# Kernel tuning notes

Hardware: AMD Instinct MI355X
Metric: run time of the kernel (lower is better)

The kernel has to match this reference:

```python
import jax, jax.numpy as jnp
import numpy as np

D_MODEL = 1024
N_HEADS = 16
HEAD_DIM = 64
N_KV_HEADS = 4
D_FF = 4096
LN_EPS = 1e-5


def setup_inputs() -> dict:
    key = jax.random.key(0)
    ks = jax.random.split(key, 10)
    s = lambda fan_in: 1.0 / np.sqrt(fan_in)
    return {
        "x": jax.random.normal(ks[0], (2, 2048, D_MODEL), dtype=jnp.float32),
        "ln_w": jnp.ones((D_MODEL,), dtype=jnp.float32),
        "ln_b": jnp.zeros((D_MODEL,), dtype=jnp.float32),
        # Linear weights stored as (in, out): y = x @ W
        "wq": jax.random.normal(ks[1], (D_MODEL, N_HEADS * HEAD_DIM), dtype=jnp.float32) * s(D_MODEL),
        "wk": jax.random.normal(ks[2], (D_MODEL, N_KV_HEADS * HEAD_DIM), dtype=jnp.float32) * s(D_MODEL),
        "wv": jax.random.normal(ks[3], (D_MODEL, N_KV_HEADS * HEAD_DIM), dtype=jnp.float32) * s(D_MODEL),
        "wo": jax.random.normal(ks[4], (N_HEADS * HEAD_DIM, D_MODEL), dtype=jnp.float32) * s(N_HEADS * HEAD_DIM),
        "w_gate": jax.random.normal(ks[5], (D_MODEL, D_FF), dtype=jnp.float32) * s(D_MODEL),
        "w_up": jax.random.normal(ks[6], (D_MODEL, D_FF), dtype=jnp.float32) * s(D_MODEL),
        "w_down": jax.random.normal(ks[7], (D_FF, D_MODEL), dtype=jnp.float32) * s(D_FF),
    }


def _layernorm(x, w, b):
    mu = jnp.mean(x, axis=-1, keepdims=True)
    var = jnp.var(x, axis=-1, keepdims=True)
    return (x - mu) * jax.lax.rsqrt(var + LN_EPS) * w + b


def _attention(normed, wq, wk, wv, wo):
    B, S, _ = normed.shape
    h, kh, hd = N_HEADS, N_KV_HEADS, HEAD_DIM
    groups = h // kh
    scale = 1.0 / np.sqrt(hd)
    q = (normed @ wq).reshape(B, S, h, hd).transpose(0, 2, 1, 3)   # [B,h,S,hd]
    k = (normed @ wk).reshape(B, S, kh, hd).transpose(0, 2, 1, 3)  # [B,kh,S,hd]
    v = (normed @ wv).reshape(B, S, kh, hd).transpose(0, 2, 1, 3)
    if groups != 1:
        # matches torch repeat_interleave along head dim
        k = jnp.repeat(k, groups, axis=1)
        v = jnp.repeat(v, groups, axis=1)
    scores = jnp.einsum("bhqd,bhkd->bhqk", q, k) * scale
    causal = jnp.tril(jnp.ones((S, S), dtype=bool))
    scores = jnp.where(causal, scores, -jnp.inf)
    attn = jax.nn.softmax(scores, axis=-1)
    out = jnp.einsum("bhqk,bhkd->bhqd", attn, v)
    out = out.transpose(0, 2, 1, 3).reshape(B, S, h * hd)
    return out @ wo


def _ffn(normed, w_gate, w_up, w_down):
    return (jax.nn.silu(normed @ w_gate) * (normed @ w_up)) @ w_down


def reference(x, ln_w, ln_b, wq, wk, wv, wo, w_gate, w_up, w_down):
    normed = _layernorm(x, ln_w, ln_b)
    attn_out = _attention(normed, wq, wk, wv, wo)
    ffn_out = _ffn(normed, w_gate, w_up, w_down)
    return x + attn_out + ffn_out
```

## Files before the change

kernel.cpp:

```cpp
#include <hip/hip_runtime.h>
#include <cstdint>

typedef __bf16 bf16x8 __attribute__((ext_vector_type(8)));
typedef float f32x4 __attribute__((ext_vector_type(4)));
typedef float f32x16 __attribute__((ext_vector_type(16)));
typedef unsigned short u16;

#define MFMA16(a, b, c) __builtin_amdgcn_mfma_f32_16x16x32_bf16((a), (b), (c), 0, 0, 0)
#define MFMA32(a, b, c) __builtin_amdgcn_mfma_f32_32x32x16_bf16((a), (b), (c), 0, 0, 0)

#define GLLDS(gp, lp) __builtin_amdgcn_global_load_lds( \
    (const __attribute__((address_space(1))) uint32_t*)(gp), \
    (__attribute__((address_space(3))) uint32_t*)(lp), 16, 0, 0)

__device__ __forceinline__ u16 f2bf(float f) {
    union { float f; uint32_t u; } v; v.f = f;
    uint32_t u = v.u;
    u += 0x7FFFu + ((u >> 16) & 1u);
    return (u16)(u >> 16);
}
__device__ __forceinline__ float bf2f(u16 h) {
    union { uint32_t u; float f; } v; v.u = ((uint32_t)h) << 16;
    return v.f;
}

__global__ __launch_bounds__(256) void transpose_cast(const float* __restrict__ in,
                                                      u16* __restrict__ out, int R, int C) {
    __shared__ float tile[32][33];
    int c0 = blockIdx.x * 32, r0 = blockIdx.y * 32;
    int tx = threadIdx.x & 31, ty = threadIdx.x >> 5;
#pragma unroll
    for (int i = ty; i < 32; i += 8)
        tile[i][tx] = in[(size_t)(r0 + i) * C + c0 + tx];
    __syncthreads();
#pragma unroll
    for (int i = ty; i < 32; i += 8)
        out[(size_t)(c0 + i) * R + r0 + tx] = f2bf(tile[tx][i]);
}

__global__ __launch_bounds__(256) void transpose_v(const u16* __restrict__ in, u16* __restrict__ out,
                                                   int in_stride) {
    __shared__ u16 tile[32][33];
    int b = blockIdx.z;
    int c0 = blockIdx.x * 32, s0 = blockIdx.y * 32;
    int tx = threadIdx.x & 31, ty = threadIdx.x >> 5;
#pragma unroll
    for (int i = ty; i < 32; i += 8)
        tile[i][tx] = in[(size_t)(b * 2048 + s0 + i) * in_stride + c0 + tx];
    __syncthreads();
#pragma unroll
    for (int i = ty; i < 32; i += 8)
        out[(size_t)b * 256 * 2048 + (size_t)(c0 + i) * 2048 + s0 + tx] = tile[tx][i];
}

__global__ __launch_bounds__(256) void ln_kernel(const float* __restrict__ x,
                                                 const float* __restrict__ w,
                                                 const float* __restrict__ bb,
                                                 u16* __restrict__ normed) {
    int row = blockIdx.x;
    int tid = threadIdx.x;
    float4 v = ((const float4*)(x + (size_t)row * 1024))[tid];
    float s = v.x + v.y + v.z + v.w;
    float s2 = v.x * v.x + v.y * v.y + v.z * v.z + v.w * v.w;
#pragma unroll
    for (int off = 1; off < 64; off <<= 1) {
        s += __shfl_xor(s, off);
        s2 += __shfl_xor(s2, off);
    }
    __shared__ float rs[4], rs2[4];
    int wv = tid >> 6;
    if ((tid & 63) == 0) { rs[wv] = s; rs2[wv] = s2; }
    __syncthreads();
    s = rs[0] + rs[1] + rs[2] + rs[3];
    s2 = rs2[0] + rs2[1] + rs2[2] + rs2[3];
    float mu = s * (1.0f / 1024.0f);
    float var = s2 * (1.0f / 1024.0f) - mu * mu;
    float inv = rsqrtf(var + 1e-5f);
    float4 wv4 = ((const float4*)w)[tid];
    float4 bv4 = ((const float4*)bb)[tid];
    ushort4 o;
    o.x = f2bf((v.x - mu) * inv * wv4.x + bv4.x);
    o.y = f2bf((v.y - mu) * inv * wv4.y + bv4.y);
    o.z = f2bf((v.z - mu) * inv * wv4.z + bv4.z);
    o.w = f2bf((v.w - mu) * inv * wv4.w + bv4.w);
    *(ushort4*)(normed + (size_t)row * 1024 + tid * 4) = o;
}

__global__ __launch_bounds__(256) void gemm_bt64(const u16* __restrict__ A, const u16* __restrict__ Bt,
                                                 void* __restrict__ Cv,
                                                 const float* __restrict__ xres,
                                                 int N, int K, int mode) {
    __shared__ __align__(16) u16 As[128 * 64];
    __shared__ __align__(16) u16 Bs[64 * 64];
    const int tid = threadIdx.x, lane = tid & 63, wv = tid >> 6;
    const int row0 = blockIdx.x * 128, col0 = blockIdx.y * 64;
    const int wr = (wv >> 1) * 64, wc = (wv & 1) * 32;
    const int fr = lane & 15, fg = lane >> 4;
    const int lr8 = lane >> 3;
    const int lc8s = ((lane & 7) ^ lr8) * 8;

    f32x4 acc[4][2];
#pragma unroll
    for (int i = 0; i < 4; ++i)
#pragma unroll
        for (int j = 0; j < 2; ++j) acc[i][j] = (f32x4){0.f, 0.f, 0.f, 0.f};

    const u16* ga = A + (size_t)(row0 + 32 * wv + lr8) * K + lc8s;
    const u16* gb = Bt + (size_t)(col0 + 16 * wv + lr8) * K + lc8s;
    u16* la = As + wv * 2048;
    u16* lb = Bs + wv * 1024;
    const int f7 = fr & 7;

    for (int k0 = 0; k0 < K; k0 += 64) {
        __syncthreads();
        GLLDS(ga + k0, la);
        GLLDS(ga + (size_t)8 * K + k0, la + 512);
        GLLDS(ga + (size_t)16 * K + k0, la + 1024);
        GLLDS(ga + (size_t)24 * K + k0, la + 1536);
        GLLDS(gb + k0, lb);
        GLLDS(gb + (size_t)8 * K + k0, lb + 512);
        __syncthreads();
#pragma unroll
        for (int kk = 0; kk < 2; ++kk) {
            bf16x8 af[4], bfr[2];
#pragma unroll
            for (int i = 0; i < 4; ++i)
                af[i] = *(const bf16x8*)(As + (wr + i * 16 + fr) * 64 + (((kk * 4 + fg) ^ f7) * 8));
#pragma unroll
            for (int j = 0; j < 2; ++j)
                bfr[j] = *(const bf16x8*)(Bs + (wc + j * 16 + fr) * 64 + (((kk * 4 + fg) ^ f7) * 8));
#pragma unroll
            for (int i = 0; i < 4; ++i)
#pragma unroll
                for (int j = 0; j < 2; ++j)
                    acc[i][j] = MFMA16(af[i], bfr[j], acc[i][j]);
        }
    }

    if (mode == 0) {
        u16* C = (u16*)Cv;
#pragma unroll
        for (int i = 0; i < 4; ++i)
#pragma unroll
            for (int j = 0; j < 2; ++j)
#pragma unroll
                for (int r = 0; r < 4; ++r) {
                    int row = row0 + wr + i * 16 + fg * 4 + r;
                    int col = col0 + wc + j * 16 + fr;
                    C[(size_t)row * N + col] = f2bf(acc[i][j][r]);
                }
    } else if (mode == 1) {
        float* C = (float*)Cv;
#pragma unroll
        for (int i = 0; i < 4; ++i)
#pragma unroll
            for (int j = 0; j < 2; ++j)
#pragma unroll
                for (int r = 0; r < 4; ++r) {
                    int row = row0 + wr + i * 16 + fg * 4 + r;
                    int col = col0 + wc + j * 16 + fr;
                    C[(size_t)row * N + col] = acc[i][j][r];
                }
    } else {
        float* C = (float*)Cv;
#pragma unroll
        for (int i = 0; i < 4; ++i)
#pragma unroll
            for (int j = 0; j < 2; ++j)
#pragma unroll
                for (int r = 0; r < 4; ++r) {
                    int row = row0 + wr + i * 16 + fg * 4 + r;
                    int col = col0 + wc + j * 16 + fr;
                    size_t off = (size_t)row * N + col;
                    C[off] = acc[i][j][r] + xres[off];
                }
    }
}

__global__ __launch_bounds__(256) void gemm_gateup(const u16* __restrict__ A,
                                                   const u16* __restrict__ Bg,
                                                   const u16* __restrict__ Bu,
                                                   u16* __restrict__ H, int N, int K) {
    __shared__ __align__(16) u16 As[128 * 64];
    __shared__ __align__(16) u16 Bgs[64 * 64];
    __shared__ __align__(16) u16 Bus[64 * 64];
    const int tid = threadIdx.x, lane = tid & 63, wv = tid >> 6;
    const int row0 = blockIdx.x * 128, col0 = blockIdx.y * 64;
    const int wr = (wv >> 1) * 64, wc = (wv & 1) * 32;
    const int fr = lane & 15, fg = lane >> 4;
    const int lr8 = lane >> 3;
    const int lc8s = ((lane & 7) ^ lr8) * 8;

    f32x4 ag[4][2], au[4][2];
#pragma unroll
    for (int i = 0; i < 4; ++i)
#pragma unroll
        for (int j = 0; j < 2; ++j) {
            ag[i][j] = (f32x4){0.f, 0.f, 0.f, 0.f};
            au[i][j] = (f32x4){0.f, 0.f, 0.f, 0.f};
        }

    const u16* ga = A + (size_t)(row0 + 32 * wv + lr8) * K + lc8s;
    const u16* gg = Bg + (size_t)(col0 + 16 * wv + lr8) * K + lc8s;
    const u16* gu = Bu + (size_t)(col0 + 16 * wv + lr8) * K + lc8s;
    u16* la = As + wv * 2048;
    u16* lg = Bgs + wv * 1024;
    u16* lu = Bus + wv * 1024;
    const int f7 = fr & 7;

    for (int k0 = 0; k0 < K; k0 += 64) {
        __syncthreads();
        GLLDS(ga + k0, la);
        GLLDS(ga + (size_t)8 * K + k0, la + 512);
        GLLDS(ga + (size_t)16 * K + k0, la + 1024);
        GLLDS(ga + (size_t)24 * K + k0, la + 1536);
        GLLDS(gg + k0, lg);
        GLLDS(gg + (size_t)8 * K + k0, lg + 512);
        GLLDS(gu + k0, lu);
        GLLDS(gu + (size_t)8 * K + k0, lu + 512);
        __syncthreads();
#pragma unroll
        for (int kk = 0; kk < 2; ++kk) {
            bf16x8 af[4], bg[2], bu[2];
#pragma unroll
            for (int i = 0; i < 4; ++i)
                af[i] = *(const bf16x8*)(As + (wr + i * 16 + fr) * 64 + (((kk * 4 + fg) ^ f7) * 8));
#pragma unroll
            for (int j = 0; j < 2; ++j) {
                bg[j] = *(const bf16x8*)(Bgs + (wc + j * 16 + fr) * 64 + (((kk * 4 + fg) ^ f7) * 8));
                bu[j] = *(const bf16x8*)(Bus + (wc + j * 16 + fr) * 64 + (((kk * 4 + fg) ^ f7) * 8));
            }
#pragma unroll
            for (int i = 0; i < 4; ++i)
#pragma unroll
                for (int j = 0; j < 2; ++j) {
                    ag[i][j] = MFMA16(af[i], bg[j], ag[i][j]);
                    au[i][j] = MFMA16(af[i], bu[j], au[i][j]);
                }
        }
    }

#pragma unroll
    for (int i = 0; i < 4; ++i)
#pragma unroll
        for (int j = 0; j < 2; ++j)
#pragma unroll
            for (int r = 0; r < 4; ++r) {
                int row = row0 + wr + i * 16 + fg * 4 + r;
                int col = col0 + wc + j * 16 + fr;
                float g = ag[i][j][r];
                float sg = g / (1.0f + __expf(-g));
                H[(size_t)row * N + col] = f2bf(sg * au[i][j][r]);
            }
}

__global__ __launch_bounds__(512) void attn_kernel(const u16* __restrict__ qkv,
                                                   const u16* __restrict__ Vt,
                                                   u16* __restrict__ Ob) {
    __shared__ __align__(16) u16 Ks[2][64 * 64];
    __shared__ __align__(16) u16 Vs[2][64 * 64];
    const int tid = threadIdx.x, lane = tid & 63, w = tid >> 6;
    const int bid = blockIdx.x;
    const int qblk = 7 - (bid & 7);
    const int h = (bid >> 3) & 15;
    const int b = bid >> 7;
    const int kh = h >> 2;
    const int q0 = qblk * 256;
    const int lo = lane & 31, hi = lane >> 5;
    const int qg = q0 + w * 32 + lo;
    const int S = 2048, QS = 1536;

    bf16x8 qf[4];
    {
        const u16* qrow = qkv + (size_t)(b * S + qg) * QS + h * 64 + 8 * hi;
        qf[0] = *(const bf16x8*)(qrow);
        qf[1] = *(const bf16x8*)(qrow + 16);
        qf[2] = *(const bf16x8*)(qrow + 32);
        qf[3] = *(const bf16x8*)(qrow + 48);
    }

    f32x16 o0 = {}, o1 = {};
    float mr = -1e30f, ls = 0.f;
    const int nt = (q0 >> 6) + 4;
    const int wq0 = q0 + w * 32;

    const int sr = w * 8 + (lane >> 3);
    const int scb = ((lane & 7) ^ (sr & 7)) * 8;
    const u16* kg = qkv + (size_t)b * S * QS + 1024 + kh * 64 + scb;
    const u16* vg = Vt + (size_t)(b * 4 + kh) * 64 * 2048 + (size_t)sr * 2048 + scb;
    u16* lk = (u16*)Ks + w * 512;
    u16* lv = (u16*)Vs + w * 512;

#define STAGE(buf, t) { const int kv0s = (t) * 64; \
    GLLDS(kg + (size_t)(kv0s + sr) * QS, lk + (buf) * 4096); \
    GLLDS(vg + kv0s, lv + (buf) * 4096); }

    STAGE(0, 0)
    asm volatile("s_waitcnt vmcnt(0)" ::: "memory");
    __syncthreads();

    const int lrow = lo * 64;
    const int l7 = lo & 7;

    for (int t = 0; t < nt; ++t) {
        const int cur = t & 1;
        if (t + 1 < nt) STAGE(cur ^ 1, t + 1)
        const int kv0 = t * 64;
        if (kv0 <= wq0 + 31) {
            const u16* KB = (const u16*)Ks + cur * 4096;
            const u16* VB = (const u16*)Vs + cur * 4096;
            f32x16 sc0 = {}, sc1 = {};
#pragma unroll
            for (int ds = 0; ds < 4; ++ds) {
                bf16x8 kf0 = *(const bf16x8*)(KB + lrow + (((2 * ds + hi) ^ l7) * 8));
                sc0 = MFMA32(kf0, qf[ds], sc0);
                bf16x8 kf1 = *(const bf16x8*)(KB + 2048 + lrow + (((2 * ds + hi) ^ l7) * 8));
                sc1 = MFMA32(kf1, qf[ds], sc1);
            }

            float xv[32];
            if (kv0 + 63 <= wq0) {
#pragma unroll
                for (int i = 0; i < 16; ++i) {
                    xv[i] = sc0[i] * 0.125f;
                    xv[16 + i] = sc1[i] * 0.125f;
                }
            } else {
#pragma unroll
                for (int i = 0; i < 16; ++i) {
                    int k0g = kv0 + (i & 3) + 8 * (i >> 2) + 4 * hi;
                    xv[i]      = (k0g      <= qg) ? sc0[i] * 0.125f : -1e30f;
                    xv[16 + i] = (k0g + 32 <= qg) ? sc1[i] * 0.125f : -1e30f;
                }
            }
            float m = xv[0];
#pragma unroll
            for (int i = 1; i < 32; ++i) m = fmaxf(m, xv[i]);
            m = fmaxf(m, __shfl_xor(m, 32));
            float nm = fmaxf(mr, m);
            float al = __expf(mr - nm);
            mr = nm;
            float sum = 0.f;
#pragma unroll
            for (int i = 0; i < 32; ++i) {
                float p = __expf(xv[i] - nm);
                xv[i] = p;
                sum += p;
            }
            sum += __shfl_xor(sum, 32);
            ls = ls * al + sum;
#pragma unroll
            for (int i = 0; i < 16; ++i) { o0[i] *= al; o1[i] *= al; }

            bf16x8 pf[4];
#pragma unroll
            for (int g = 0; g < 4; ++g) {
                uint32_t w0, w1, w2, w3;
                asm("v_cvt_pk_bf16_f32 %0, %1, %2" : "=v"(w0) : "v"(xv[g * 8 + 0]), "v"(xv[g * 8 + 1]));
                asm("v_cvt_pk_bf16_f32 %0, %1, %2" : "=v"(w1) : "v"(xv[g * 8 + 2]), "v"(xv[g * 8 + 3]));
                asm("v_cvt_pk_bf16_f32 %0, %1, %2" : "=v"(w2) : "v"(xv[g * 8 + 4]), "v"(xv[g * 8 + 5]));
                asm("v_cvt_pk_bf16_f32 %0, %1, %2" : "=v"(w3) : "v"(xv[g * 8 + 6]), "v"(xv[g * 8 + 7]));
                asm volatile("v_permlane32_swap_b32 %0, %1" : "+v"(w0), "+v"(w2));
                asm volatile("v_permlane32_swap_b32 %0, %1" : "+v"(w1), "+v"(w3));
                union { uint32_t u[4]; bf16x8 v; } pk;
                pk.u[0] = w0; pk.u[1] = w1; pk.u[2] = w2; pk.u[3] = w3;
                pf[g] = pk.v;
            }

#pragma unroll
            for (int ks = 0; ks < 4; ++ks) {
                bf16x8 vf0 = *(const bf16x8*)(VB + lrow + (((2 * ks + hi) ^ l7) * 8));
                o0 = MFMA32(vf0, pf[ks], o0);
                bf16x8 vf1 = *(const bf16x8*)(VB + 2048 + lrow + (((2 * ks + hi) ^ l7) * 8));
                o1 = MFMA32(vf1, pf[ks], o1);
            }
        }
        asm volatile("s_waitcnt vmcnt(0)" ::: "memory");
        __syncthreads();
    }
#undef STAGE

    const float inv = 1.0f / ls;
    u16* orow = Ob + (size_t)(b * S + qg) * 1024 + h * 64;
#pragma unroll
    for (int rg = 0; rg < 4; ++rg) {
        ushort4 w4;
        w4.x = f2bf(o0[rg * 4 + 0] * inv);
        w4.y = f2bf(o0[rg * 4 + 1] * inv);
        w4.z = f2bf(o0[rg * 4 + 2] * inv);
        w4.w = f2bf(o0[rg * 4 + 3] * inv);
        *(ushort4*)(orow + rg * 8 + 4 * hi) = w4;
        w4.x = f2bf(o1[rg * 4 + 0] * inv);
        w4.y = f2bf(o1[rg * 4 + 1] * inv);
        w4.z = f2bf(o1[rg * 4 + 2] * inv);
        w4.w = f2bf(o1[rg * 4 + 3] * inv);
        *(ushort4*)(orow + 32 + rg * 8 + 4 * hi) = w4;
    }
}

extern "C" void kernel_launch(void* const* d_in, const int* in_sizes, int n_in,
                              void* d_out, int out_size, void* d_ws, size_t ws_size,
                              hipStream_t stream) {
    const float* x    = (const float*)d_in[0];
    const float* ln_w = (const float*)d_in[1];
    const float* ln_b = (const float*)d_in[2];
    const float* wq   = (const float*)d_in[3];
    const float* wk   = (const float*)d_in[4];
    const float* wv   = (const float*)d_in[5];
    const float* wo   = (const float*)d_in[6];
    const float* wg   = (const float*)d_in[7];
    const float* wu   = (const float*)d_in[8];
    const float* wd   = (const float*)d_in[9];
    float* out = (float*)d_out;

    char* ws = (char*)d_ws;
    u16* QKVT   = (u16*)(ws + 0x0000000);
    u16* WOT    = (u16*)(ws + 0x0300000);
    u16* WGT    = (u16*)(ws + 0x0500000);
    u16* WUT    = (u16*)(ws + 0x0D00000);
    u16* WDT    = (u16*)(ws + 0x1500000);
    u16* NORMED = (u16*)(ws + 0x1D00000);
    u16* QKV    = (u16*)(ws + 0x2500000);
    u16* VT     = (u16*)(ws + 0x3100000);
    u16* ATTN   = (u16*)(ws + 0x3300000);
    float* P1   = (float*)(ws + 0x3B00000);
    u16* Hb     = (u16*)(ws + 0x4B00000);

    transpose_cast<<<dim3(32, 32), 256, 0, stream>>>(wq, QKVT, 1024, 1024);
    transpose_cast<<<dim3(8, 32), 256, 0, stream>>>(wk, QKVT + (size_t)1024 * 1024, 1024, 256);
    transpose_cast<<<dim3(8, 32), 256, 0, stream>>>(wv, QKVT + (size_t)1280 * 1024, 1024, 256);
    transpose_cast<<<dim3(32, 32), 256, 0, stream>>>(wo, WOT, 1024, 1024);
    transpose_cast<<<dim3(128, 32), 256, 0, stream>>>(wg, WGT, 1024, 4096);
    transpose_cast<<<dim3(128, 32), 256, 0, stream>>>(wu, WUT, 1024, 4096);
    transpose_cast<<<dim3(32, 128), 256, 0, stream>>>(wd, WDT, 4096, 1024);

    ln_kernel<<<4096, 256, 0, stream>>>(x, ln_w, ln_b, NORMED);

    gemm_bt64<<<dim3(32, 24), 256, 0, stream>>>(NORMED, QKVT, QKV, nullptr, 1536, 1024, 0);
    transpose_v<<<dim3(8, 64, 2), 256, 0, stream>>>(QKV + 1280, VT, 1536);
    attn_kernel<<<256, 512, 0, stream>>>(QKV, VT, ATTN);
    gemm_bt64<<<dim3(32, 16), 256, 0, stream>>>(ATTN, WOT, P1, x, 1024, 1024, 4);

    gemm_gateup<<<dim3(32, 64), 256, 0, stream>>>(NORMED, WGT, WUT, Hb, 4096, 1024);
    gemm_bt64<<<dim3(32, 16), 256, 0, stream>>>(Hb, WDT, out, P1, 1024, 4096, 4);
}
```

Baseline: 290.2 us.

## Interleave gate/up weights and use 256x256 double-buffered 8-wave gate-up GEMM

Gate and up weights are transposed into one interleaved matrix (16-column groups alternating gate/up), so a single B stream feeds both products. The gate-up GEMM becomes a 256x256 tile, 512-thread kernel with double-buffered LDS, prefetch split across phases, and setprio around MFMA bursts. The aim is more data reuse per tile and overlap of global loads with compute. In exchange it uses much more LDS and registers (128 accumulator floats per lane) and launches only 512 blocks, which limits occupancy.

```diff
diff --git a/kernel.cpp b/kernel.cpp
--- a/kernel.cpp
+++ b/kernel.cpp
@@ -36,6 +36,23 @@
 #pragma unroll
     for (int i = ty; i < 32; i += 8)
         out[(size_t)(c0 + i) * R + r0 + tx] = f2bf(tile[tx][i]);
+}
+
+__global__ __launch_bounds__(256) void transpose_cast_gu(const float* __restrict__ in,
+                                                         u16* __restrict__ out, int upflag) {
+    __shared__ float tile[32][33];
+    int c0 = blockIdx.x * 32, r0 = blockIdx.y * 32;
+    int tx = threadIdx.x & 31, ty = threadIdx.x >> 5;
+#pragma unroll
+    for (int i = ty; i < 32; i += 8)
+        tile[i][tx] = in[(size_t)(r0 + i) * 4096 + c0 + tx];
+    __syncthreads();
+#pragma unroll
+    for (int i = ty; i < 32; i += 8) {
+        int n = c0 + i;
+        int orow = ((n >> 4) << 5) + (n & 15) + upflag * 16;
+        out[(size_t)orow * 1024 + r0 + tx] = f2bf(tile[tx][i]);
+    }
 }
 
 __global__ __launch_bounds__(256) void transpose_v(const u16* __restrict__ in, u16* __restrict__ out,
@@ -177,80 +194,126 @@
     }
 }
 
-__global__ __launch_bounds__(256) void gemm_gateup(const u16* __restrict__ A,
-                                                   const u16* __restrict__ Bg,
-                                                   const u16* __restrict__ Bu,
-                                                   u16* __restrict__ H, int N, int K) {
-    __shared__ __align__(16) u16 As[128 * 64];
-    __shared__ __align__(16) u16 Bgs[64 * 64];
-    __shared__ __align__(16) u16 Bus[64 * 64];
-    const int tid = threadIdx.x, lane = tid & 63, wv = tid >> 6;
-    const int row0 = blockIdx.x * 128, col0 = blockIdx.y * 64;
-    const int wr = (wv >> 1) * 64, wc = (wv & 1) * 32;
-    const int fr = lane & 15, fg = lane >> 4;
-    const int lr8 = lane >> 3;
-    const int lc8s = ((lane & 7) ^ lr8) * 8;
-
-    f32x4 ag[4][2], au[4][2];
-#pragma unroll
-    for (int i = 0; i < 4; ++i)
-#pragma unroll
-        for (int j = 0; j < 2; ++j) {
-            ag[i][j] = (f32x4){0.f, 0.f, 0.f, 0.f};
-            au[i][j] = (f32x4){0.f, 0.f, 0.f, 0.f};
+__global__ __launch_bounds__(512, 2) void gemm_wgu_8ph(const u16* __restrict__ A,
+                                                       const u16* __restrict__ Bp,
+                                                       u16* __restrict__ H) {
+    __shared__ __align__(16) u16 As[2][256 * 64];
+    __shared__ __align__(16) u16 Bs[2][256 * 64];
+    const int tid = threadIdx.x, lane = tid & 63, w = tid >> 6;
+    const int wm = w >> 2, wn = w & 3;
+    const int row0 = blockIdx.x * 256;
+    const int col0 = blockIdx.y * 256;
+    const int fr = lane & 15, fg = lane >> 4, f7 = fr & 7;
+    const int K = 1024;
+    const int nk = 16;
+
+    f32x4 acc[8][4];
+#pragma unroll
+    for (int i = 0; i < 8; ++i)
+#pragma unroll
+        for (int j = 0; j < 4; ++j) acc[i][j] = (f32x4){0.f, 0.f, 0.f, 0.f};
+
+    const int pA = w & 3;
+    const int pB = (wn & 1) * 2 + wm;
+    const int lr = lane >> 3;
+    const int lcS = ((lane & 7) ^ lr) * 8;
+    const u16* gA = A + (size_t)(row0 + wm * 128 + pA * 32 + lr) * K + lcS;
+    const u16* gB = Bp + (size_t)(col0 + (wn >> 1) * 128 + pB * 32 + lr) * K + lcS;
+    u16* lAs = (u16*)As + (wm * 128 + pA * 32) * 64;
+    u16* lBs = (u16*)Bs + ((wn >> 1) * 128 + pB * 32) * 64;
+
+#define STAGE_A(BUF, KO) { _Pragma("unroll") for (int c = 0; c < 4; ++c) \
+    GLLDS(gA + (size_t)(c * 8) * 1024 + (KO), lAs + (BUF) * 16384 + c * 512); }
+#define STAGE_B(BUF, KO) { _Pragma("unroll") for (int c = 0; c < 4; ++c) \
+    GLLDS(gB + (size_t)(c * 8) * 1024 + (KO), lBs + (BUF) * 16384 + c * 512); }
+
+#define DSRD(rh, ch, CUR)                                                        \
+    bf16x8 af0[4], af1[4], bq0[2], bq1[2];                                       \
+    {                                                                            \
+        const u16* Ab = (const u16*)As + (CUR) * 16384;                          \
+        const u16* Bb = (const u16*)Bs + (CUR) * 16384;                          \
+        const int x0 = (fg ^ f7) * 8, x1 = ((4 + fg) ^ f7) * 8;                  \
+        _Pragma("unroll") for (int i = 0; i < 4; ++i) {                          \
+            const u16* p = Ab + (wm * 128 + (rh) * 64 + i * 16 + fr) * 64;       \
+            af0[i] = *(const bf16x8*)(p + x0);                                   \
+            af1[i] = *(const bf16x8*)(p + x1);                                   \
+        }                                                                        \
+        _Pragma("unroll") for (int j = 0; j < 2; ++j) {                          \
+            const u16* p = Bb + (wn * 64 + (ch) * 32 + j * 16 + fr) * 64;        \
+            bq0[j] = *(const bf16x8*)(p + x0);                                   \
+            bq1[j] = *(const bf16x8*)(p + x1);                                   \
+        }                                                                        \
+    }
+#define MM(rh, ch)                                                               \
+    __builtin_amdgcn_s_setprio(1);                                               \
+    _Pragma("unroll") for (int i = 0; i < 4; ++i)                                \
+        _Pragma("unroll") for (int j = 0; j < 2; ++j) {                          \
+            acc[(rh)*4+i][(ch)*2+j] = MFMA16(af0[i], bq0[j], acc[(rh)*4+i][(ch)*2+j]); \
+            acc[(rh)*4+i][(ch)*2+j] = MFMA16(af1[i], bq1[j], acc[(rh)*4+i][(ch)*2+j]); \
+        }                                                                        \
+    __builtin_amdgcn_s_setprio(0);
+#define BAR asm volatile("s_barrier" ::: "memory")
+
+    STAGE_A(0, 0)
+    STAGE_B(0, 0)
+    asm volatile("s_waitcnt vmcnt(0)" ::: "memory");
+    BAR;
+
+    for (int t = 0; t < nk; ++t) {
+        const int cur = t & 1, nxt = cur ^ 1;
+        const int kn = (t + 1) * 64;
+        const bool pf = (t + 1 < nk);
+        {
+            DSRD(0, 0, cur)
+            if (pf) STAGE_A(nxt, kn)
+            BAR;
+            MM(0, 0)
+            BAR;
         }
-
-    const u16* ga = A + (size_t)(row0 + 32 * wv + lr8) * K + lc8s;
-    const u16* gg = Bg + (size_t)(col0 + 16 * wv + lr8) * K + lc8s;
-    const u16* gu = Bu + (size_t)(col0 + 16 * wv + lr8) * K + lc8s;
-    u16* la = As + wv * 2048;
-    u16* lg = Bgs + wv * 1024;
-    u16* lu = Bus + wv * 1024;
-    const int f7 = fr & 7;
-
-    for (int k0 = 0; k0 < K; k0 += 64) {
-        __syncthreads();
-        GLLDS(ga + k0, la);
-        GLLDS(ga + (size_t)8 * K + k0, la + 512);
-        GLLDS(ga + (size_t)16 * K + k0, la + 1024);
-        GLLDS(ga + (size_t)24 * K + k0, la + 1536);
-        GLLDS(gg + k0, lg);
-        GLLDS(gg + (size_t)8 * K + k0, lg + 512);
-        GLLDS(gu + k0, lu);
-        GLLDS(gu + (size_t)8 * K + k0, lu + 512);
-        __syncthreads();
-#pragma unroll
-        for (int kk = 0; kk < 2; ++kk) {
-            bf16x8 af[4], bg[2], bu[2];
-#pragma unroll
-            for (int i = 0; i < 4; ++i)
-                af[i] = *(const bf16x8*)(As + (wr + i * 16 + fr) * 64 + (((kk * 4 + fg) ^ f7) * 8));
-#pragma unroll
-            for (int j = 0; j < 2; ++j) {
-                bg[j] = *(const bf16x8*)(Bgs + (wc + j * 16 + fr) * 64 + (((kk * 4 + fg) ^ f7) * 8));
-                bu[j] = *(const bf16x8*)(Bus + (wc + j * 16 + fr) * 64 + (((kk * 4 + fg) ^ f7) * 8));
-            }
-#pragma unroll
-            for (int i = 0; i < 4; ++i)
-#pragma unroll
-                for (int j = 0; j < 2; ++j) {
-                    ag[i][j] = MFMA16(af[i], bg[j], ag[i][j]);
-                    au[i][j] = MFMA16(af[i], bu[j], au[i][j]);
+        {
+            DSRD(1, 0, cur)
+            if (pf) STAGE_B(nxt, kn)
+            BAR;
+            MM(1, 0)
+            BAR;
+        }
+        {
+            DSRD(0, 1, cur)
+            BAR;
+            MM(0, 1)
+            BAR;
+        }
+        {
+            DSRD(1, 1, cur)
+            BAR;
+            MM(1, 1)
+            asm volatile("s_waitcnt vmcnt(0)" ::: "memory");
+            BAR;
+        }
+    }
+#undef STAGE_A
+#undef STAGE_B
+#undef DSRD
+#undef MM
+#undef BAR
+
+#pragma unroll
+    for (int rh = 0; rh < 2; ++rh)
+#pragma unroll
+        for (int i = 0; i < 4; ++i)
+#pragma unroll
+            for (int ch = 0; ch < 2; ++ch) {
+                f32x4 g = acc[rh * 4 + i][ch * 2];
+                f32x4 u = acc[rh * 4 + i][ch * 2 + 1];
+                int G = (col0 + wn * 64 + ch * 32) >> 5;
+                int hcol = G * 16 + fr;
+                int hrow = row0 + wm * 128 + rh * 64 + i * 16 + fg * 4;
+#pragma unroll
+                for (int r = 0; r < 4; ++r) {
+                    float gg = g[r];
+                    float sg = gg / (1.0f + __expf(-gg));
+                    H[(size_t)(hrow + r) * 4096 + hcol] = f2bf(sg * u[r]);
                 }
-        }
-    }
-
-#pragma unroll
-    for (int i = 0; i < 4; ++i)
-#pragma unroll
-        for (int j = 0; j < 2; ++j)
-#pragma unroll
-            for (int r = 0; r < 4; ++r) {
-                int row = row0 + wr + i * 16 + fg * 4 + r;
-                int col = col0 + wc + j * 16 + fr;
-                float g = ag[i][j][r];
-                float sg = g / (1.0f + __expf(-g));
-                H[(size_t)row * N + col] = f2bf(sg * au[i][j][r]);
             }
 }
 
@@ -416,8 +479,7 @@
     char* ws = (char*)d_ws;
     u16* QKVT   = (u16*)(ws + 0x0000000);
     u16* WOT    = (u16*)(ws + 0x0300000);
-    u16* WGT    = (u16*)(ws + 0x0500000);
-    u16* WUT    = (u16*)(ws + 0x0D00000);
+    u16* WGU    = (u16*)(ws + 0x0500000);
     u16* WDT    = (u16*)(ws + 0x1500000);
     u16* NORMED = (u16*)(ws + 0x1D00000);
     u16* QKV    = (u16*)(ws + 0x2500000);
@@ -430,8 +492,8 @@
     transpose_cast<<<dim3(8, 32), 256, 0, stream>>>(wk, QKVT + (size_t)1024 * 1024, 1024, 256);
     transpose_cast<<<dim3(8, 32), 256, 0, stream>>>(wv, QKVT + (size_t)1280 * 1024, 1024, 256);
     transpose_cast<<<dim3(32, 32), 256, 0, stream>>>(wo, WOT, 1024, 1024);
-    transpose_cast<<<dim3(128, 32), 256, 0, stream>>>(wg, WGT, 1024, 4096);
-    transpose_cast<<<dim3(128, 32), 256, 0, stream>>>(wu, WUT, 1024, 4096);
+    transpose_cast_gu<<<dim3(128, 32), 256, 0, stream>>>(wg, WGU, 0);
+    transpose_cast_gu<<<dim3(128, 32), 256, 0, stream>>>(wu, WGU, 1);
     transpose_cast<<<dim3(32, 128), 256, 0, stream>>>(wd, WDT, 4096, 1024);
 
     ln_kernel<<<4096, 256, 0, stream>>>(x, ln_w, ln_b, NORMED);
@@ -441,6 +503,6 @@
     attn_kernel<<<256, 512, 0, stream>>>(QKV, VT, ATTN);
     gemm_bt64<<<dim3(32, 16), 256, 0, stream>>>(ATTN, WOT, P1, x, 1024, 1024, 4);
 
-    gemm_gateup<<<dim3(32, 64), 256, 0, stream>>>(NORMED, WGT, WUT, Hb, 4096, 1024);
+    gemm_wgu_8ph<<<dim3(16, 32), 512, 0, stream>>>(NORMED, WGU, Hb);
     gemm_bt64<<<dim3(32, 16), 256, 0, stream>>>(Hb, WDT, out, P1, 1024, 4096, 4);
 }
```

After: 287.3 us. About the same (-1.0%).

## Interleave gate/up weights and triple-buffer gate-up GEMM with larger tiles

Applied to the files above, without the earlier changes.

The gate and up weights are transposed into one interleaved matrix, with alternating 16-row groups of gate and up columns, so a single B tile holds both halves. The gate-up GEMM becomes a 512-thread, 256x128 tile kernel with a three-stage global-to-LDS prefetch pipeline, explicit vmcnt waits, s_setprio around the MFMA blocks, and the SiLU*up epilogue fused in. The aim is to hide load latency behind compute and raise data reuse per block. The cost is more LDS use (144 KB) and registers, which limits occupancy to one block per CU.

```diff
diff --git a/kernel.cpp b/kernel.cpp
--- a/kernel.cpp
+++ b/kernel.cpp
@@ -36,6 +36,23 @@
 #pragma unroll
     for (int i = ty; i < 32; i += 8)
         out[(size_t)(c0 + i) * R + r0 + tx] = f2bf(tile[tx][i]);
+}
+
+__global__ __launch_bounds__(256) void transpose_cast_gu(const float* __restrict__ in,
+                                                         u16* __restrict__ out, int upflag) {
+    __shared__ float tile[32][33];
+    int c0 = blockIdx.x * 32, r0 = blockIdx.y * 32;
+    int tx = threadIdx.x & 31, ty = threadIdx.x >> 5;
+#pragma unroll
+    for (int i = ty; i < 32; i += 8)
+        tile[i][tx] = in[(size_t)(r0 + i) * 4096 + c0 + tx];
+    __syncthreads();
+#pragma unroll
+    for (int i = ty; i < 32; i += 8) {
+        int n = c0 + i;
+        int orow = ((n >> 4) << 5) + (n & 15) + upflag * 16;
+        out[(size_t)orow * 1024 + r0 + tx] = f2bf(tile[tx][i]);
+    }
 }
 
 __global__ __launch_bounds__(256) void transpose_v(const u16* __restrict__ in, u16* __restrict__ out,
@@ -177,81 +194,81 @@
     }
 }
 
-__global__ __launch_bounds__(256) void gemm_gateup(const u16* __restrict__ A,
-                                                   const u16* __restrict__ Bg,
-                                                   const u16* __restrict__ Bu,
-                                                   u16* __restrict__ H, int N, int K) {
-    __shared__ __align__(16) u16 As[128 * 64];
-    __shared__ __align__(16) u16 Bgs[64 * 64];
-    __shared__ __align__(16) u16 Bus[64 * 64];
-    const int tid = threadIdx.x, lane = tid & 63, wv = tid >> 6;
-    const int row0 = blockIdx.x * 128, col0 = blockIdx.y * 64;
-    const int wr = (wv >> 1) * 64, wc = (wv & 1) * 32;
-    const int fr = lane & 15, fg = lane >> 4;
-    const int lr8 = lane >> 3;
-    const int lc8s = ((lane & 7) ^ lr8) * 8;
-
-    f32x4 ag[4][2], au[4][2];
-#pragma unroll
-    for (int i = 0; i < 4; ++i)
-#pragma unroll
-        for (int j = 0; j < 2; ++j) {
-            ag[i][j] = (f32x4){0.f, 0.f, 0.f, 0.f};
-            au[i][j] = (f32x4){0.f, 0.f, 0.f, 0.f};
+__global__ __launch_bounds__(512, 1) void gemm_wgu_3buf(const u16* __restrict__ A,
+                                                        const u16* __restrict__ Bp,
+                                                        u16* __restrict__ H) {
+    __shared__ __align__(16) u16 As[3 * 256 * 64];
+    __shared__ __align__(16) u16 Bs[3 * 128 * 64];
+    const int tid = threadIdx.x, lane = tid & 63, w = tid >> 6;
+    const int wm = w >> 2, wn = w & 3;
+    const int row0 = blockIdx.x * 256;
+    const int colb0 = blockIdx.y * 128;
+    const int fr = lane & 15, fg = lane >> 4, f7 = fr & 7;
+    const int K = 1024, nk = 16;
+
+    f32x4 acc[8][2];
+#pragma unroll
+    for (int i = 0; i < 8; ++i)
+#pragma unroll
+        for (int j = 0; j < 2; ++j) acc[i][j] = (f32x4){0.f, 0.f, 0.f, 0.f};
+
+    const int lr = lane >> 3;
+    const int lcS = ((lane & 7) ^ lr) * 8;
+    const u16* gA = A + (size_t)(row0 + w * 32 + lr) * K + lcS;
+    const u16* gB = Bp + (size_t)(colb0 + w * 16 + lr) * K + lcS;
+    u16* lA = (u16*)As + w * 2048;
+    u16* lB = (u16*)Bs + w * 1024;
+
+#define STG(BUF, KO) { \
+    _Pragma("unroll") for (int g = 0; g < 4; ++g) \
+        GLLDS(gA + (size_t)(g * 8) * K + (KO), lA + (BUF) * 16384 + g * 512); \
+    _Pragma("unroll") for (int g = 0; g < 2; ++g) \
+        GLLDS(gB + (size_t)(g * 8) * K + (KO), lB + (BUF) * 8192 + g * 512); }
+
+    STG(0, 0)
+    STG(1, 64)
+    asm volatile("s_waitcnt vmcnt(6)" ::: "memory");
+    asm volatile("s_barrier" ::: "memory");
+
+    for (int t = 0; t < nk; ++t) {
+        if (t + 2 < nk) STG((t + 2) % 3, (t + 2) * 64)
+        const u16* Ab = (const u16*)As + (t % 3) * 16384;
+        const u16* Bb = (const u16*)Bs + (t % 3) * 8192;
+#pragma unroll
+        for (int kk = 0; kk < 2; ++kk) {
+            const int xo = ((kk * 4 + fg) ^ f7) * 8;
+            bf16x8 af[8], bq[2];
+#pragma unroll
+            for (int i = 0; i < 8; ++i)
+                af[i] = *(const bf16x8*)(Ab + (wm * 128 + i * 16 + fr) * 64 + xo);
+#pragma unroll
+            for (int j = 0; j < 2; ++j)
+                bq[j] = *(const bf16x8*)(Bb + (wn * 32 + j * 16 + fr) * 64 + xo);
+            __builtin_amdgcn_s_setprio(1);
+#pragma unroll
+            for (int i = 0; i < 8; ++i)
+#pragma unroll
+                for (int j = 0; j < 2; ++j)
+                    acc[i][j] = MFMA16(af[i], bq[j], acc[i][j]);
+            __builtin_amdgcn_s_setprio(0);
         }
-
-    const u16* ga = A + (size_t)(row0 + 32 * wv + lr8) * K + lc8s;
-    const u16* gg = Bg + (size_t)(col0 + 16 * wv + lr8) * K + lc8s;
-    const u16* gu = Bu + (size_t)(col0 + 16 * wv + lr8) * K + lc8s;
-    u16* la = As + wv * 2048;
-    u16* lg = Bgs + wv * 1024;
-    u16* lu = Bus + wv * 1024;
-    const int f7 = fr & 7;
-
-    for (int k0 = 0; k0 < K; k0 += 64) {
-        __syncthreads();
-        GLLDS(ga + k0, la);
-        GLLDS(ga + (size_t)8 * K + k0, la + 512);
-        GLLDS(ga + (size_t)16 * K + k0, la + 1024);
-        GLLDS(ga + (size_t)24 * K + k0, la + 1536);
-        GLLDS(gg + k0, lg);
-        GLLDS(gg + (size_t)8 * K + k0, lg + 512);
-        GLLDS(gu + k0, lu);
-        GLLDS(gu + (size_t)8 * K + k0, lu + 512);
-        __syncthreads();
-#pragma unroll
-        for (int kk = 0; kk < 2; ++kk) {
-            bf16x8 af[4], bg[2], bu[2];
-#pragma unroll
-            for (int i = 0; i < 4; ++i)
-                af[i] = *(const bf16x8*)(As + (wr + i * 16 + fr) * 64 + (((kk * 4 + fg) ^ f7) * 8));
-#pragma unroll
-            for (int j = 0; j < 2; ++j) {
-                bg[j] = *(const bf16x8*)(Bgs + (wc + j * 16 + fr) * 64 + (((kk * 4 + fg) ^ f7) * 8));
-                bu[j] = *(const bf16x8*)(Bus + (wc + j * 16 + fr) * 64 + (((kk * 4 + fg) ^ f7) * 8));
-            }
-#pragma unroll
-            for (int i = 0; i < 4; ++i)
-#pragma unroll
-                for (int j = 0; j < 2; ++j) {
-                    ag[i][j] = MFMA16(af[i], bg[j], ag[i][j]);
-                    au[i][j] = MFMA16(af[i], bu[j], au[i][j]);
-                }
+        if (t + 2 < nk) { asm volatile("s_waitcnt vmcnt(6)" ::: "memory"); }
+        else            { asm volatile("s_waitcnt vmcnt(0)" ::: "memory"); }
+        asm volatile("s_barrier" ::: "memory");
+    }
+#undef STG
+
+    const int hc = ((colb0 >> 5) + wn) * 16 + fr;
+#pragma unroll
+    for (int i = 0; i < 8; ++i) {
+        int hrow = row0 + wm * 128 + i * 16 + fg * 4;
+#pragma unroll
+        for (int r = 0; r < 4; ++r) {
+            float g = acc[i][0][r];
+            float sg = g / (1.0f + __expf(-g));
+            H[(size_t)(hrow + r) * 4096 + hc] = f2bf(sg * acc[i][1][r]);
         }
     }
-
-#pragma unroll
-    for (int i = 0; i < 4; ++i)
-#pragma unroll
-        for (int j = 0; j < 2; ++j)
-#pragma unroll
-            for (int r = 0; r < 4; ++r) {
-                int row = row0 + wr + i * 16 + fg * 4 + r;
-                int col = col0 + wc + j * 16 + fr;
-                float g = ag[i][j][r];
-                float sg = g / (1.0f + __expf(-g));
-                H[(size_t)row * N + col] = f2bf(sg * au[i][j][r]);
-            }
 }
 
 __global__ __launch_bounds__(512) void attn_kernel(const u16* __restrict__ qkv,
@@ -416,8 +433,7 @@
     char* ws = (char*)d_ws;
     u16* QKVT   = (u16*)(ws + 0x0000000);
     u16* WOT    = (u16*)(ws + 0x0300000);
-    u16* WGT    = (u16*)(ws + 0x0500000);
-    u16* WUT    = (u16*)(ws + 0x0D00000);
+    u16* WGU    = (u16*)(ws + 0x0500000);
     u16* WDT    = (u16*)(ws + 0x1500000);
     u16* NORMED = (u16*)(ws + 0x1D00000);
     u16* QKV    = (u16*)(ws + 0x2500000);
@@ -430,8 +446,8 @@
     transpose_cast<<<dim3(8, 32), 256, 0, stream>>>(wk, QKVT + (size_t)1024 * 1024, 1024, 256);
     transpose_cast<<<dim3(8, 32), 256, 0, stream>>>(wv, QKVT + (size_t)1280 * 1024, 1024, 256);
     transpose_cast<<<dim3(32, 32), 256, 0, stream>>>(wo, WOT, 1024, 1024);
-    transpose_cast<<<dim3(128, 32), 256, 0, stream>>>(wg, WGT, 1024, 4096);
-    transpose_cast<<<dim3(128, 32), 256, 0, stream>>>(wu, WUT, 1024, 4096);
+    transpose_cast_gu<<<dim3(128, 32), 256, 0, stream>>>(wg, WGU, 0);
+    transpose_cast_gu<<<dim3(128, 32), 256, 0, stream>>>(wu, WGU, 1);
     transpose_cast<<<dim3(32, 128), 256, 0, stream>>>(wd, WDT, 4096, 1024);
 
     ln_kernel<<<4096, 256, 0, stream>>>(x, ln_w, ln_b, NORMED);
@@ -441,6 +457,6 @@
     attn_kernel<<<256, 512, 0, stream>>>(QKV, VT, ATTN);
     gemm_bt64<<<dim3(32, 16), 256, 0, stream>>>(ATTN, WOT, P1, x, 1024, 1024, 4);
 
-    gemm_gateup<<<dim3(32, 64), 256, 0, stream>>>(NORMED, WGT, WUT, Hb, 4096, 1024);
+    gemm_wgu_3buf<<<dim3(16, 64), 512, 0, stream>>>(NORMED, WGU, Hb);
     gemm_bt64<<<dim3(32, 16), 256, 0, stream>>>(Hb, WDT, out, P1, 1024, 4096, 4);
 }
```

Result: slower. 312.1 us (+7.6%).
